# Kernel optimization log

Measured on AMD Instinct MI355X. Metric: run time of the kernel, lower is better.

## Reference

```python
import jax, jax.numpy as jnp
import numpy as np

N_ATOMS = 10000
N_PAIRS = 320000
C = 64        # channel width (pp_nodes[-1], ii_nodes[-1], pi_nodes[-1])
NB = 10       # n_basis
EPS = 1e-3    # torsion-boost epsilon


def setup_inputs() -> dict:
    key = jax.random.key(0)
    ks = jax.random.split(key, 24)
    f32 = jnp.float32

    def w(k, shp):
        return jax.random.normal(k, shp, f32) / np.float32(np.sqrt(shp[0]))

    ind_2 = jax.random.randint(ks[0], (N_PAIRS, 2), 0, N_ATOMS)
    p1 = jax.random.normal(ks[1], (N_ATOMS, C), f32)
    p3 = jax.random.normal(ks[2], (N_ATOMS, 3, C), f32)
    basis = jax.random.uniform(ks[3], (N_PAIRS, NB), dtype=f32)
    d3 = jax.random.normal(ks[4], (N_PAIRS, 3), f32)
    d3 = d3 / jnp.linalg.norm(d3, axis=-1, keepdims=True)  # unit bond directions
    fc_edge = jax.random.uniform(ks[5], (N_PAIRS, 1), dtype=f32)  # cutoff in [0,1]

    return {
        'ind_2': ind_2, 'p1': p1, 'p3': p3, 'basis': basis, 'd3': d3, 'fc_edge': fc_edge,
        'pp_pre_W1': w(ks[6], (C, C)), 'pp_pre_b1': jnp.zeros((C,), f32),
        'pp_pre_W2': w(ks[7], (C, C)), 'pp_pre_b2': jnp.zeros((C,), f32),
        'pi_W': w(ks[8], (2 * C, C * NB)), 'pi_b': jnp.zeros((C * NB,), f32),
        'ii_W': w(ks[9], (C, 2 * C)),
        'pp_post_W1': w(ks[10], (2 * C, C)), 'pp_post_W2': w(ks[11], (C, C)),
        'eq_pp_W': w(ks[12], (C, C)),
        'pp1_W1': w(ks[13], (2 * C, C)), 'pp1_b1': jnp.zeros((C,), f32),
        'pp1_W2': w(ks[14], (C, 2 * C)), 'pp1_b2': jnp.zeros((2 * C,), f32),
    }


def _gc_block(ind_2, p1, p3, basis, d3, fc_edge,
              pp_pre_W1, pp_pre_b1, pp_pre_W2, pp_pre_b2,
              pi_W, pi_b, ii_W, pp_post_W1, pp_post_W2,
              eq_pp_W, pp1_W1, pp1_b1, pp1_W2, pp1_b2):
    n_atoms = p1.shape[0]
    i = ind_2[:, 0]
    j = ind_2[:, 1]

    # ---- InvarLayer ----
    # pp_pre: FF [C,C], tanh, bias
    p1_in = jnp.tanh(jnp.tanh(p1 @ pp_pre_W1 + pp_pre_b1) @ pp_pre_W2 + pp_pre_b2)
    # PILayer: concat(p1[i], p1[j]) -> Dense(C*NB) -> contract with radial basis
    pair = jnp.concatenate([p1_in[i], p1_in[j]], axis=-1)            # (P, 2C)
    h = jnp.tanh(pair @ pi_W + pi_b).reshape(-1, C, NB)              # (P, C, NB)
    i_pair = jnp.einsum('pcb,pb->pc', h, basis)                      # (P, C)
    # ii: FF [2C] (doubled for n_props=2), tanh, no bias
    i_pair = jnp.tanh(i_pair @ ii_W)                                 # (P, 2C)
    # IP: scatter-add onto receiver atom i
    p1_scat = jax.ops.segment_sum(i_pair, i, num_segments=n_atoms)   # (N, 2C)
    # pp_post: FF [C,C], tanh, no bias
    p1_new = jnp.tanh(jnp.tanh(p1_scat @ pp_post_W1) @ pp_post_W2)   # (N, C)

    i1a, i1b = jnp.split(i_pair, 2, axis=-1)  # chunks; rank-3 branch uses i1s[1]

    # ---- torsion boost (compute_torsion_boost_t3) ----
    v = jax.ops.segment_sum(d3 * fc_edge, i, num_segments=n_atoms)   # (N, 3)
    v_i = v[i]
    proj = jnp.sum(v_i * d3, axis=-1, keepdims=True)
    w = v_i - proj * d3                                              # perpendicular part
    w2 = jnp.sum(w * w, axis=-1, keepdims=True)
    g_deg = w2 / (w2 + (10.0 * EPS) ** 2)
    t3 = w * jax.lax.rsqrt(w2 + EPS * EPS) * g_deg                   # (P, 3)
    tb_gate = g_deg * (fc_edge * fc_edge)                            # (P, 1)

    # ---- EquivarLayer ----
    gate = i1b[:, None, :]                                           # (P, 1, C)
    ix = p3[j] * gate + d3[:, :, None] * gate \
         + t3[:, :, None] * (i1b * tb_gate)[:, None, :]              # (P, 3, C)
    p3_new = jax.ops.segment_sum(ix, i, num_segments=n_atoms)        # (N, 3, C)
    p3_new = p3_new @ eq_pp_W                                        # PP: no bias, no act
    dotted = jnp.einsum('ixr,ixr->ir', p3_new, p3_new)               # (N, C)

    # ---- output PP + gating ----
    h2 = jnp.tanh(jnp.concatenate([p1_new, dotted], axis=-1) @ pp1_W1 + pp1_b1)
    h2 = jnp.tanh(h2 @ pp1_W2 + pp1_b2)                              # (N, 2C)
    g1, g3 = jnp.split(h2, 2, axis=-1)
    p1_out = g1                                                      # (N, C)
    p3_out = p3_new * g3[:, None, :]                                 # ScaleLayer
    return p1_out, p3_out


def reference(ind_2, p1, p3, basis, d3, fc_edge,
              pp_pre_W1, pp_pre_b1, pp_pre_W2, pp_pre_b2,
              pi_W, pi_b, ii_W, pp_post_W1, pp_post_W2,
              eq_pp_W, pp1_W1, pp1_b1, pp1_W2, pp1_b2):
    return _gc_block(ind_2, p1, p3, basis, d3, fc_edge,
                     pp_pre_W1, pp_pre_b1, pp_pre_W2, pp_pre_b2,
                     pi_W, pi_b, ii_W, pp_post_W1, pp_post_W2,
                     eq_pp_W, pp1_W1, pp1_b1, pp1_W2, pp1_b2)
```

## Files before the change

### kernel.cpp

```cpp
#include <hip/hip_runtime.h>
#include <hip/hip_bf16.h>

#define N_ATOMS 10000
#define N_PAIRS 320000
#define C_ 64
#define NB_ 10

typedef short bf16x8 __attribute__((ext_vector_type(8)));
typedef float f32x4 __attribute__((ext_vector_type(4)));

__device__ __forceinline__ float bf2f(__hip_bfloat16 x) { return __bfloat162float(x); }
__device__ __forceinline__ float ldf(const void* p, int i, int isf32) {
    return isf32 ? ((const float*)p)[i] : bf2f(((const __hip_bfloat16*)p)[i]);
}
__device__ __forceinline__ short f2bs(float x) {
    __hip_bfloat16 h = __float2bfloat16(x);
    return *reinterpret_cast<short*>(&h);
}
__device__ __forceinline__ float bs2f(unsigned short s) {
    return __uint_as_float(((unsigned)s) << 16);
}
__device__ __forceinline__ float tanh_fast(float x) {
    const float e = __expf(2.0f * x);
    return 1.0f - 2.0f * __builtin_amdgcn_rcpf(e + 1.0f);
}

#define W_PPREW1 0
#define W_PPREB1 4096
#define W_PPREW2 4160
#define W_PPREB2 8256
#define W_PIW    8320
#define W_PIB    90240
#define W_IIW    90880
#define W_PPOSTW1 99072
#define W_PPOSTW2 107264
#define W_EQW    111360
#define W_Q1W    115456
#define W_Q1B    123648
#define W_Q2W    123712
#define W_Q2B    131904
#define W_TOTAL  132032

__global__ void k_probe(const void* __restrict__ d3, int* __restrict__ flag)
{
    if (threadIdx.x == 0 && blockIdx.x == 0) {
        float sf = 0.f, sb = 0.f;
        const float* f = (const float*)d3;
        const __hip_bfloat16* b = (const __hip_bfloat16*)d3;
        for (int r = 0; r < 4; r++) {
            float x = f[r*3], y = f[r*3+1], z = f[r*3+2];
            float n = x*x + y*y + z*z;
            sf += isfinite(n) ? fabsf(n - 1.f) : 1e30f;
            float xb = bf2f(b[r*3]), yb = bf2f(b[r*3+1]), zb = bf2f(b[r*3+2]);
            float nb = xb*xb + yb*yb + zb*zb;
            sb += isfinite(nb) ? fabsf(nb - 1.f) : 1e30f;
        }
        *flag = (sf < sb) ? 1 : 0;
    }
}

__global__ __launch_bounds__(256) void k_convert(
    const void* s0, const void* s1, const void* s2, const void* s3,
    const void* s4, const void* s5, const void* s6, const void* s7,
    const void* s8, const void* s9, const void* s10, const void* s11,
    const void* s12, const void* s13,
    float* __restrict__ wbuf, const int* __restrict__ flagp)
{
    const int idx = blockIdx.x * 256 + threadIdx.x;
    if (idx >= W_TOTAL) return;
    const int isf32 = *flagp;
    const int offs[15] = {W_PPREW1, W_PPREB1, W_PPREW2, W_PPREB2, W_PIW, W_PIB,
                          W_IIW, W_PPOSTW1, W_PPOSTW2, W_EQW, W_Q1W, W_Q1B,
                          W_Q2W, W_Q2B, W_TOTAL};
    const void* srcs[14] = {s0,s1,s2,s3,s4,s5,s6,s7,s8,s9,s10,s11,s12,s13};
    int t = 0;
    while (idx >= offs[t + 1]) t++;
    wbuf[idx] = ldf(srcs[t], idx - offs[t], isf32);
}

__global__ __launch_bounds__(256) void k_pack(
    const float* __restrict__ wbuf,
    short* __restrict__ piWBh, short* __restrict__ piWBl,
    short* __restrict__ iiWh, short* __restrict__ iiWl)
{
    int idx = blockIdx.x * 256 + threadIdx.x;
    if (idx < 81920) {
        const int j = idx & 7, lane = (idx >> 3) & 63, s = (idx >> 9) & 3, T = idx >> 11;
        const int k = s * 32 + (lane >> 4) * 8 + j;
        const int colp = T * 16 + (lane & 15);
        const int b = colp >> 6, c = colp & 63;
        const float v = wbuf[W_PIW + k * 640 + c * 10 + b];
        const short hs = f2bs(v);
        piWBh[idx] = hs;
        piWBl[idx] = f2bs(v - bs2f((unsigned short)hs));
        return;
    }
    idx -= 81920;
    if (idx < 8192) {
        const int j = idx & 7, lane = (idx >> 3) & 63, s2 = (idx >> 9) & 1, ct = idx >> 10;
        const int k = s2 * 32 + (lane >> 4) * 8 + j;
        const int col = ct * 16 + (lane & 15);
        const float wv = wbuf[W_IIW + k * 128 + col];
        const short hs = f2bs(wv);
        iiWh[idx] = hs;
        iiWl[idx] = f2bs(wv - bs2f((unsigned short)hs));
    }
}

__global__ __launch_bounds__(256) void k_p1in(
    const void* __restrict__ p1, const float* __restrict__ wbuf,
    const int* __restrict__ flagp,
    unsigned short* __restrict__ p1h, unsigned short* __restrict__ p1l)
{
    const float* W1 = wbuf + W_PPREW1;
    const float* b1 = wbuf + W_PPREB1;
    const float* W2 = wbuf + W_PPREW2;
    const float* b2 = wbuf + W_PPREB2;
    const int isf32 = *flagp;
    __shared__ float x[4][C_];
    __shared__ float h[4][C_];
    const int t = threadIdx.x;
    const int slot = t >> 6, c = t & 63;
    const int atom = blockIdx.x * 4 + slot;
    x[slot][c] = ldf(p1, atom * C_ + c, isf32);
    __syncthreads();
    float acc = b1[c];
    for (int k = 0; k < C_; k++) acc += x[slot][k] * W1[k * C_ + c];
    h[slot][c] = tanh_fast(acc);
    __syncthreads();
    acc = b2[c];
    for (int k = 0; k < C_; k++) acc += h[slot][k] * W2[k * C_ + c];
    const float f = tanh_fast(acc);
    const short hs = f2bs(f);
    p1h[atom * C_ + c] = (unsigned short)hs;
    p1l[atom * C_ + c] = (unsigned short)f2bs(f - bs2f((unsigned short)hs));
}

__global__ __launch_bounds__(256) void k_hist(const int* __restrict__ ind2, int* __restrict__ cnt)
{
    const int p = blockIdx.x * 256 + threadIdx.x;
    if (p < N_PAIRS) atomicAdd(&cnt[ind2[2 * p]], 1);
}
__global__ __launch_bounds__(256) void k_scan(const int* __restrict__ cnt, int* __restrict__ offs)
{
    __shared__ int part[256];
    __shared__ int base[257];
    const int t = threadIdx.x;
    const int lo = t * 40, hi = (lo + 40 < N_ATOMS) ? lo + 40 : N_ATOMS;
    int s = 0;
    for (int b = lo; b < hi; b++) s += cnt[b];
    part[t] = s;
    __syncthreads();
    if (t == 0) {
        int run = 0;
        for (int i = 0; i < 256; i++) { base[i] = run; run += part[i]; }
        base[256] = run;
    }
    __syncthreads();
    int run = base[t];
    for (int b = lo; b < hi; b++) { offs[b] = run; run += cnt[b]; }
    if (t == 0) offs[N_ATOMS] = base[256];
}
__global__ __launch_bounds__(256) void k_cpcur(const int* __restrict__ offs, int* __restrict__ cur)
{
    const int i = blockIdx.x * 256 + threadIdx.x;
    if (i < N_ATOMS) cur[i] = offs[i];
}
__global__ __launch_bounds__(256) void k_scatter(const int* __restrict__ ind2,
                                                 int* __restrict__ cur, int* __restrict__ perm)
{
    const int p = blockIdx.x * 256 + threadIdx.x;
    if (p >= N_PAIRS) return;
    const int pos = atomicAdd(&cur[ind2[2 * p]], 1);
    perm[pos] = p;
}

__global__ __launch_bounds__(256) void k_vscat(
    const int* __restrict__ ind2, const void* __restrict__ d3,
    const void* __restrict__ fc, const int* __restrict__ flagp, float* __restrict__ v)
{
    const int p = blockIdx.x * 256 + threadIdx.x;
    if (p >= N_PAIRS) return;
    const int isf32 = *flagp;
    const int ia = ind2[2 * p];
    const float f = ldf(fc, p, isf32);
    atomicAdd(&v[ia * 3 + 0], ldf(d3, p * 3 + 0, isf32) * f);
    atomicAdd(&v[ia * 3 + 1], ldf(d3, p * 3 + 1, isf32) * f);
    atomicAdd(&v[ia * 3 + 2], ldf(d3, p * 3 + 2, isf32) * f);
}

template<int FULLMODE>
__global__ __launch_bounds__(256) void k_pairs_t(
    const int* __restrict__ ind2, const void* __restrict__ basis,
    const void* __restrict__ d3, const void* __restrict__ fc,
    const void* __restrict__ p3,
    const float* __restrict__ wbuf,
    const short* __restrict__ piWBh, const short* __restrict__ piWBl,
    const short* __restrict__ iiWh, const short* __restrict__ iiWl,
    const unsigned short* __restrict__ p1h, const unsigned short* __restrict__ p1l,
    const int* __restrict__ flagp, const float* __restrict__ vglob,
    float* __restrict__ outA, float* __restrict__ outB)
{
    __shared__ __align__(16) unsigned short Bbuf[8192];
    __shared__ __align__(16) char SH[17408];
    __shared__ float basisL[640];
    __shared__ int sIL[64], sJL[64];
    __shared__ float d3L[64][3], t3L[64][3], tbL[64];

    float* preL = (float*)SH;
    float* i1bL = (float*)SH;

    const int t = threadIdx.x;
    const int P0 = blockIdx.x * 64;
    const int isf32 = *flagp;
    const int lane = t & 63;
    const int w = t >> 6;
    const int lc = lane & 15;
    const int quad = lane >> 4;

    if (t < 64) {
        int2 ij = ((const int2*)ind2)[P0 + t];
        sIL[t] = ij.x; sJL[t] = ij.y;
    }
    for (int e = t; e < 640; e += 256) basisL[e] = ldf(basis, P0 * 10 + e, isf32);
    __syncthreads();

    bf16x8 ah[4], al[4];
    {
        const int ia = sIL[w * 16 + lc];
        const int ja = sJL[w * 16 + lc];
        #pragma unroll
        for (int s = 0; s < 4; s++) {
            const int atom = (s < 2) ? ia : ja;
            const int off = atom * 64 + (s & 1) * 32 + quad * 8;
            ah[s] = *(const bf16x8*)(p1h + off);
            al[s] = *(const bf16x8*)(p1l + off);
        }
    }

    float sr[4][4];
    #pragma unroll
    for (int r = 0; r < 4; r++)
        #pragma unroll
        for (int ph = 0; ph < 4; ph++) sr[r][ph] = 0.f;

    for (int cc = 0; cc < 10; cc++) {
        f32x4 acc[4];
        #pragma unroll
        for (int tt = 0; tt < 4; tt++) acc[tt] = (f32x4){0.f, 0.f, 0.f, 0.f};

        __syncthreads();
        {
            const uint4* gsrc = (const uint4*)(piWBh + cc * 8192);
            uint4* ldst = (uint4*)Bbuf;
            #pragma unroll
            for (int r = 0; r < 4; r++) ldst[r * 256 + t] = gsrc[r * 256 + t];
        }
        __syncthreads();
        #pragma unroll
        for (int tt = 0; tt < 4; tt++) {
            #pragma unroll
            for (int s = 0; s < 4; s++) {
                bf16x8 bfr = *(const bf16x8*)&Bbuf[((tt * 4 + s) * 64 + lane) * 8];
                acc[tt] = __builtin_amdgcn_mfma_f32_16x16x32_bf16(ah[s], bfr, acc[tt], 0, 0, 0);
                acc[tt] = __builtin_amdgcn_mfma_f32_16x16x32_bf16(al[s], bfr, acc[tt], 0, 0, 0);
            }
        }
        __syncthreads();
        {
            const uint4* gsrc = (const uint4*)(piWBl + cc * 8192);
            uint4* ldst = (uint4*)Bbuf;
            #pragma unroll
            for (int r = 0; r < 4; r++) ldst[r * 256 + t] = gsrc[r * 256 + t];
        }
        __syncthreads();
        #pragma unroll
        for (int tt = 0; tt < 4; tt++) {
            #pragma unroll
            for (int s = 0; s < 4; s++) {
                bf16x8 bfr = *(const bf16x8*)&Bbuf[((tt * 4 + s) * 64 + lane) * 8];
                acc[tt] = __builtin_amdgcn_mfma_f32_16x16x32_bf16(ah[s], bfr, acc[tt], 0, 0, 0);
            }
            const int c = tt * 16 + lc;
            const float bias = wbuf[W_PIB + c * 10 + cc];
            #pragma unroll
            for (int r = 0; r < 4; r++) {
                const int m = w * 16 + quad * 4 + r;
                const float h = tanh_fast(acc[tt][r] + bias);
                sr[r][tt] += h * basisL[m * 10 + cc];
            }
        }
    }

    #pragma unroll
    for (int r = 0; r < 4; r++)
        #pragma unroll
        for (int ph = 0; ph < 4; ph++)
            preL[(w * 16 + quad * 4 + r) * 68 + ph * 16 + lc] = sr[r][ph];
    __syncthreads();

    bf16x8 ah2[2], al2[2];
    {
        const int row = w * 16 + lc;
        #pragma unroll
        for (int s2 = 0; s2 < 2; s2++) {
            const float* pr2 = &preL[row * 68 + s2 * 32 + quad * 8];
            #pragma unroll
            for (int j = 0; j < 8; j++) {
                const float x = pr2[j];
                const short hs = f2bs(x);
                ah2[s2][j] = hs;
                al2[s2][j] = f2bs(x - bs2f((unsigned short)hs));
            }
        }
    }
    __syncthreads();

    #pragma unroll
    for (int ct = 0; ct < 8; ct++) {
        f32x4 acc = {0.f, 0.f, 0.f, 0.f};
        #pragma unroll
        for (int s2 = 0; s2 < 2; s2++) {
            bf16x8 bh = *(const bf16x8*)&iiWh[((ct * 2 + s2) * 64 + lane) * 8];
            bf16x8 bl = *(const bf16x8*)&iiWl[((ct * 2 + s2) * 64 + lane) * 8];
            acc = __builtin_amdgcn_mfma_f32_16x16x32_bf16(ah2[s2], bh, acc, 0, 0, 0);
            acc = __builtin_amdgcn_mfma_f32_16x16x32_bf16(al2[s2], bh, acc, 0, 0, 0);
            acc = __builtin_amdgcn_mfma_f32_16x16x32_bf16(ah2[s2], bl, acc, 0, 0, 0);
        }
        const int ch = ct * 16 + lc;
        if (FULLMODE) {
            #pragma unroll
            for (int r = 0; r < 4; r++) {
                const int m = w * 16 + quad * 4 + r;
                outA[(size_t)(P0 + m) * 128 + ch] = tanh_fast(acc[r]);
            }
        } else {
            #pragma unroll
            for (int r = 0; r < 4; r++) {
                const int m = w * 16 + quad * 4 + r;
                const float val = tanh_fast(acc[r]);
                atomicAdd(&outA[(size_t)sIL[m] * 128 + ch], val);
                if (ch >= 64) i1bL[m * 64 + (ch - 64)] = val;
            }
        }
    }

    if (!FULLMODE) {
        __syncthreads();
        if (t < 64) {
            const int m = t;
            const int ia = sIL[m];
            const float vi0 = vglob[ia * 3 + 0], vi1 = vglob[ia * 3 + 1], vi2 = vglob[ia * 3 + 2];
            const float d0 = ldf(d3, (P0 + m) * 3 + 0, isf32);
            const float d1 = ldf(d3, (P0 + m) * 3 + 1, isf32);
            const float d2 = ldf(d3, (P0 + m) * 3 + 2, isf32);
            d3L[m][0] = d0; d3L[m][1] = d1; d3L[m][2] = d2;
            const float proj = vi0 * d0 + vi1 * d1 + vi2 * d2;
            const float w0 = vi0 - proj * d0, w1 = vi1 - proj * d1, w2v = vi2 - proj * d2;
            const float w2 = w0 * w0 + w1 * w1 + w2v * w2v;
            const float g = w2 / (w2 + 1e-4f);
            const float rs = rsqrtf(w2 + 1e-6f);
            t3L[m][0] = w0 * rs * g; t3L[m][1] = w1 * rs * g; t3L[m][2] = w2v * rs * g;
            const float f = ldf(fc, P0 + m, isf32);
            tbL[m] = g * f * f;
        }
        __syncthreads();
        const int c = lane;
        #pragma unroll 4
        for (int mm = 0; mm < 16; mm++) {
            const int m = w * 16 + mm;
            const float bv = i1bL[m * 64 + c];
            const float coef = bv * tbL[m];
            #pragma unroll
            for (int x = 0; x < 3; x++) {
                const float p3v = ldf(p3, sJL[m] * 192 + x * 64 + c, isf32);
                atomicAdd(&outB[(size_t)sIL[m] * 192 + x * 64 + c],
                          p3v * bv + d3L[m][x] * bv + t3L[m][x] * coef);
            }
        }
    }
}

__global__ __launch_bounds__(64) void k_reduce(
    const int* __restrict__ ind2, const void* __restrict__ d3,
    const void* __restrict__ fc, const void* __restrict__ p3,
    const float* __restrict__ ip, const int* __restrict__ perm,
    const int* __restrict__ offs, const float* __restrict__ wbuf,
    const int* __restrict__ flagp, void* __restrict__ out)
{
    const int a = blockIdx.x;
    const int l = threadIdx.x;
    const int isf32 = *flagp;
    const int q0 = offs[a], q1 = offs[a + 1];

    float vx = 0.f, vy = 0.f, vz = 0.f;
    for (int q = q0 + l; q < q1; q += 64) {
        const int p = perm[q];
        const float f = ldf(fc, p, isf32);
        vx += ldf(d3, 3 * p + 0, isf32) * f;
        vy += ldf(d3, 3 * p + 1, isf32) * f;
        vz += ldf(d3, 3 * p + 2, isf32) * f;
    }
    #pragma unroll
    for (int off = 32; off; off >>= 1) {
        vx += __shfl_xor(vx, off);
        vy += __shfl_xor(vy, off);
        vz += __shfl_xor(vz, off);
    }

    float accA = 0.f, accB = 0.f, a30 = 0.f, a31 = 0.f, a32 = 0.f;
    #pragma unroll 2
    for (int q = q0; q < q1; q++) {
        const int p = perm[q];
        const float f = ldf(fc, p, isf32);
        const float d0 = ldf(d3, 3 * p + 0, isf32);
        const float d1 = ldf(d3, 3 * p + 1, isf32);
        const float d2 = ldf(d3, 3 * p + 2, isf32);
        const float proj = vx * d0 + vy * d1 + vz * d2;
        const float w0 = vx - proj * d0, w1 = vy - proj * d1, w2v = vz - proj * d2;
        const float w2 = w0 * w0 + w1 * w1 + w2v * w2v;
        const float g = w2 / (w2 + 1e-4f);
        const float rs = rsqrtf(w2 + 1e-6f);
        const float t30 = w0 * rs * g, t31 = w1 * rs * g, t32 = w2v * rs * g;
        const float tb = g * f * f;
        const int jj = ind2[2 * p + 1];
        const float ipa = ip[(size_t)p * 128 + l];
        const float ipb = ip[(size_t)p * 128 + 64 + l];
        accA += ipa; accB += ipb;
        const float coef = ipb * tb;
        a30 += ldf(p3, jj * 192 + l, isf32) * ipb + d0 * ipb + t30 * coef;
        a31 += ldf(p3, jj * 192 + 64 + l, isf32) * ipb + d1 * ipb + t31 * coef;
        a32 += ldf(p3, jj * 192 + 128 + l, isf32) * ipb + d2 * ipb + t32 * coef;
    }

    __shared__ float s1m[128];
    __shared__ float p3s[192];
    __shared__ float hA[64];
    __shared__ float cat[128];
    __shared__ float hB[64];
    s1m[l] = accA; s1m[64 + l] = accB;
    p3s[l] = a30; p3s[64 + l] = a31; p3s[128 + l] = a32;
    __syncthreads();

    const float* ppW1 = wbuf + W_PPOSTW1;
    const float* ppW2 = wbuf + W_PPOSTW2;
    const float* eqW  = wbuf + W_EQW;
    const float* q1W  = wbuf + W_Q1W;
    const float* q1b  = wbuf + W_Q1B;
    const float* q2W  = wbuf + W_Q2W;
    const float* q2b  = wbuf + W_Q2B;

    float acc = 0.f;
    for (int k = 0; k < 128; k++) acc += s1m[k] * ppW1[k * 64 + l];
    hA[l] = tanh_fast(acc);
    __syncthreads();
    acc = 0.f;
    for (int k = 0; k < 64; k++) acc += hA[k] * ppW2[k * 64 + l];
    const float p1n = tanh_fast(acc);

    float pn0 = 0.f, pn1 = 0.f, pn2 = 0.f;
    for (int k = 0; k < 64; k++) {
        const float e = eqW[k * 64 + l];
        pn0 += p3s[k] * e;
        pn1 += p3s[64 + k] * e;
        pn2 += p3s[128 + k] * e;
    }
    cat[l] = p1n;
    cat[64 + l] = pn0 * pn0 + pn1 * pn1 + pn2 * pn2;
    __syncthreads();

    acc = q1b[l];
    for (int k = 0; k < 128; k++) acc += cat[k] * q1W[k * 64 + l];
    hB[l] = tanh_fast(acc);
    __syncthreads();

    float g1 = q2b[l], g3 = q2b[64 + l];
    for (int k = 0; k < 64; k++) {
        const float hv = hB[k];
        g1 += hv * q2W[k * 128 + l];
        g3 += hv * q2W[k * 128 + 64 + l];
    }
    g1 = tanh_fast(g1);
    g3 = tanh_fast(g3);

    if (isf32) {
        float* p1o = (float*)out;
        float* p3o = p1o + 640000;
        p1o[a * 64 + l] = g1;
        p3o[a * 192 + l] = pn0 * g3;
        p3o[a * 192 + 64 + l] = pn1 * g3;
        p3o[a * 192 + 128 + l] = pn2 * g3;
    } else {
        __hip_bfloat16* p1o = (__hip_bfloat16*)out;
        __hip_bfloat16* p3o = p1o + 640000;
        p1o[a * 64 + l] = __float2bfloat16(g1);
        p3o[a * 192 + l] = __float2bfloat16(pn0 * g3);
        p3o[a * 192 + 64 + l] = __float2bfloat16(pn1 * g3);
        p3o[a * 192 + 128 + l] = __float2bfloat16(pn2 * g3);
    }
}

__global__ __launch_bounds__(256) void k_final(
    const float* __restrict__ p1scat, const float* __restrict__ p3acc,
    const float* __restrict__ wbuf, const int* __restrict__ flagp,
    void* __restrict__ out)
{
    const float* ppW1 = wbuf + W_PPOSTW1;
    const float* ppW2 = wbuf + W_PPOSTW2;
    const float* eqW  = wbuf + W_EQW;
    const float* q1W  = wbuf + W_Q1W;
    const float* q1b  = wbuf + W_Q1B;
    const float* q2W  = wbuf + W_Q2W;
    const float* q2b  = wbuf + W_Q2B;
    const int isf32 = *flagp;

    __shared__ float s1[4][128];
    __shared__ float hA[4][64];
    __shared__ float cat[4][128];
    __shared__ float p3a[4][192];
    const int t = threadIdx.x;
    const int slot = t >> 6, c = t & 63;
    const int atom = blockIdx.x * 4 + slot;

    s1[slot][c]        = p1scat[atom * 128 + c];
    s1[slot][64 + c]   = p1scat[atom * 128 + 64 + c];
    p3a[slot][c]       = p3acc[atom * 192 + c];
    p3a[slot][64 + c]  = p3acc[atom * 192 + 64 + c];
    p3a[slot][128 + c] = p3acc[atom * 192 + 128 + c];
    __syncthreads();

    float acc = 0.f;
    for (int k = 0; k < 128; k++) acc += s1[slot][k] * ppW1[k * 64 + c];
    hA[slot][c] = tanh_fast(acc);
    __syncthreads();
    acc = 0.f;
    for (int k = 0; k < 64; k++) acc += hA[slot][k] * ppW2[k * 64 + c];
    cat[slot][c] = tanh_fast(acc);

    float pn[3];
    float dot = 0.f;
    #pragma unroll
    for (int x = 0; x < 3; x++) {
        float a = 0.f;
        for (int k = 0; k < 64; k++) a += p3a[slot][x * 64 + k] * eqW[k * 64 + c];
        pn[x] = a;
        dot += a * a;
    }
    cat[slot][64 + c] = dot;
    __syncthreads();

    acc = q1b[c];
    for (int k = 0; k < 128; k++) acc += cat[slot][k] * q1W[k * 64 + c];
    __syncthreads();
    hA[slot][c] = tanh_fast(acc);
    __syncthreads();

    float g1acc = q2b[c], g3acc = q2b[c + 64];
    for (int k = 0; k < 64; k++) {
        const float hv = hA[slot][k];
        g1acc += hv * q2W[k * 128 + c];
        g3acc += hv * q2W[k * 128 + c + 64];
    }
    const float g1 = tanh_fast(g1acc);
    const float g3 = tanh_fast(g3acc);
    if (isf32) {
        float* p1o = (float*)out;
        float* p3o = p1o + 640000;
        p1o[atom * 64 + c] = g1;
        #pragma unroll
        for (int x = 0; x < 3; x++) p3o[atom * 192 + x * 64 + c] = pn[x] * g3;
    } else {
        __hip_bfloat16* p1o = (__hip_bfloat16*)out;
        __hip_bfloat16* p3o = p1o + 640000;
        p1o[atom * 64 + c] = __float2bfloat16(g1);
        #pragma unroll
        for (int x = 0; x < 3; x++) p3o[atom * 192 + x * 64 + c] = __float2bfloat16(pn[x] * g3);
    }
}

extern "C" void kernel_launch(void* const* d_in, const int* in_sizes, int n_in,
                              void* d_out, int out_size, void* d_ws, size_t ws_size,
                              hipStream_t stream)
{
    const int* ind2 = (const int*)d_in[0];
    const void* p1    = d_in[1];
    const void* p3    = d_in[2];
    const void* basis = d_in[3];
    const void* d3    = d_in[4];
    const void* fc    = d_in[5];

    char* W = (char*)d_ws;
    float* wbuf  = (float*)(W + 0);
    short* piWBh = (short*)(W + 528128);
    short* piWBl = (short*)(W + 691968);
    short* iiWh  = (short*)(W + 855808);
    short* iiWl  = (short*)(W + 872192);
    unsigned short* p1h = (unsigned short*)(W + 888576);
    unsigned short* p1l = (unsigned short*)(W + 2168576);
    int* flag = (int*)(W + 3448576);

    const int full = (ws_size >= 168688704ULL) ? 1 : 0;

    k_probe<<<1, 64, 0, stream>>>(d3, flag);
    k_convert<<<516, 256, 0, stream>>>(
        d_in[6], d_in[7], d_in[8], d_in[9], d_in[10], d_in[11], d_in[12],
        d_in[13], d_in[14], d_in[15], d_in[16], d_in[17], d_in[18], d_in[19],
        wbuf, flag);
    k_pack<<<352, 256, 0, stream>>>(wbuf, piWBh, piWBl, iiWh, iiWl);
    k_p1in<<<2500, 256, 0, stream>>>(p1, wbuf, flag, p1h, p1l);

    if (full) {
        int* cnt  = (int*)(W + 3448640);
        int* offs = (int*)(W + 3488640);
        int* cur  = (int*)(W + 3528704);
        int* perm = (int*)(W + 3568704);
        float* ip = (float*)(W + 4848704);

        hipMemsetAsync(cnt, 0, 40000, stream);
        k_hist<<<1250, 256, 0, stream>>>(ind2, cnt);
        k_scan<<<1, 256, 0, stream>>>(cnt, offs);
        k_cpcur<<<40, 256, 0, stream>>>(offs, cur);
        k_scatter<<<1250, 256, 0, stream>>>(ind2, cur, perm);
        k_pairs_t<1><<<5000, 256, 0, stream>>>(ind2, basis, d3, fc, p3,
                                               wbuf, piWBh, piWBl, iiWh, iiWl,
                                               p1h, p1l, flag, nullptr,
                                               ip, nullptr);
        k_reduce<<<10000, 64, 0, stream>>>(ind2, d3, fc, p3, ip, perm, offs,
                                           wbuf, flag, d_out);
    } else {
        float* v      = (float*)(W + 3448640);
        float* p1scat = (float*)(W + 3568640);
        float* p3acc  = (float*)(W + 8688640);

        hipMemsetAsync(v, 0, 120000 + 5120000 + 7680000, stream);
        k_vscat<<<1250, 256, 0, stream>>>(ind2, d3, fc, flag, v);
        k_pairs_t<0><<<5000, 256, 0, stream>>>(ind2, basis, d3, fc, p3,
                                               wbuf, piWBh, piWBl, iiWh, iiWl,
                                               p1h, p1l, flag, v,
                                               p1scat, p3acc);
        k_final<<<2500, 256, 0, stream>>>(p1scat, p3acc, wbuf, flag, d_out);
    }
}
```

Baseline: 528.3 us.

## Sort pairs by destination atom and pre-reduce runs before atomic scatter

Drops the two-mode path (full materialization plus per-atom reduce, or unsorted atomics) and always builds a counting-sort permutation of pairs by source atom. The vscat and pairs kernels process pairs in sorted order, so consecutive pairs share an atom; runs are summed in registers or shared memory and flushed with a single atomic per run instead of one per pair. This cuts atomic traffic to p1scat and p3acc and the size-dependent ip buffer, at the cost of the histogram, scan and scatter kernels and gathered reads of basis, d3 and fc through the permutation.

```diff
diff --git a/kernel.cpp b/kernel.cpp
--- a/kernel.cpp
+++ b/kernel.cpp
@@ -177,20 +177,34 @@
 
 __global__ __launch_bounds__(256) void k_vscat(
     const int* __restrict__ ind2, const void* __restrict__ d3,
-    const void* __restrict__ fc, const int* __restrict__ flagp, float* __restrict__ v)
-{
-    const int p = blockIdx.x * 256 + threadIdx.x;
-    if (p >= N_PAIRS) return;
+    const void* __restrict__ fc, const int* __restrict__ flagp,
+    const int* __restrict__ perm, float* __restrict__ v)
+{
+    __shared__ int iA[256];
+    __shared__ float sx[256], sy[256], sz[256];
+    const int t = threadIdx.x;
+    const int q = blockIdx.x * 256 + t;
     const int isf32 = *flagp;
+    const int p = perm[q];
     const int ia = ind2[2 * p];
     const float f = ldf(fc, p, isf32);
-    atomicAdd(&v[ia * 3 + 0], ldf(d3, p * 3 + 0, isf32) * f);
-    atomicAdd(&v[ia * 3 + 1], ldf(d3, p * 3 + 1, isf32) * f);
-    atomicAdd(&v[ia * 3 + 2], ldf(d3, p * 3 + 2, isf32) * f);
-}
-
-template<int FULLMODE>
-__global__ __launch_bounds__(256) void k_pairs_t(
+    iA[t] = ia;
+    sx[t] = ldf(d3, 3 * p + 0, isf32) * f;
+    sy[t] = ldf(d3, 3 * p + 1, isf32) * f;
+    sz[t] = ldf(d3, 3 * p + 2, isf32) * f;
+    __syncthreads();
+    const bool head = (t == 0) || (iA[t - 1] != ia);
+    if (head) {
+        float ax = sx[t], ay = sy[t], az = sz[t];
+        int m = t + 1;
+        while (m < 256 && iA[m] == ia) { ax += sx[m]; ay += sy[m]; az += sz[m]; m++; }
+        atomicAdd(&v[ia * 3 + 0], ax);
+        atomicAdd(&v[ia * 3 + 1], ay);
+        atomicAdd(&v[ia * 3 + 2], az);
+    }
+}
+
+__global__ __launch_bounds__(256) void k_pairs(
     const int* __restrict__ ind2, const void* __restrict__ basis,
     const void* __restrict__ d3, const void* __restrict__ fc,
     const void* __restrict__ p3,
@@ -199,16 +213,16 @@
     const short* __restrict__ iiWh, const short* __restrict__ iiWl,
     const unsigned short* __restrict__ p1h, const unsigned short* __restrict__ p1l,
     const int* __restrict__ flagp, const float* __restrict__ vglob,
-    float* __restrict__ outA, float* __restrict__ outB)
-{
-    __shared__ __align__(16) unsigned short Bbuf[8192];
-    __shared__ __align__(16) char SH[17408];
+    const int* __restrict__ perm,
+    float* __restrict__ p1scat, float* __restrict__ p3acc)
+{
+    __shared__ __align__(16) char U[33792];
+    unsigned short* Bbuf = (unsigned short*)U;
+    float* preL = (float*)(U + 16384);
+    float* ipL  = (float*)U;
     __shared__ float basisL[640];
-    __shared__ int sIL[64], sJL[64];
-    __shared__ float d3L[64][3], t3L[64][3], tbL[64];
-
-    float* preL = (float*)SH;
-    float* i1bL = (float*)SH;
+    __shared__ int pmL[64], sIL[64], sJL[64];
+    __shared__ float fcL[64], d3L[64][3], t3L[64][3], tbL[64];
 
     const int t = threadIdx.x;
     const int P0 = blockIdx.x * 64;
@@ -218,11 +232,21 @@
     const int lc = lane & 15;
     const int quad = lane >> 4;
 
+    if (t < 64) pmL[t] = perm[P0 + t];
+    __syncthreads();
     if (t < 64) {
-        int2 ij = ((const int2*)ind2)[P0 + t];
+        const int p = pmL[t];
+        int2 ij = ((const int2*)ind2)[p];
         sIL[t] = ij.x; sJL[t] = ij.y;
-    }
-    for (int e = t; e < 640; e += 256) basisL[e] = ldf(basis, P0 * 10 + e, isf32);
+        fcL[t] = ldf(fc, p, isf32);
+        d3L[t][0] = ldf(d3, 3 * p + 0, isf32);
+        d3L[t][1] = ldf(d3, 3 * p + 1, isf32);
+        d3L[t][2] = ldf(d3, 3 * p + 2, isf32);
+    }
+    for (int e = t; e < 640; e += 256) {
+        const int m = e / 10, b = e % 10;
+        basisL[e] = ldf(basis, pmL[m] * 10 + b, isf32);
+    }
     __syncthreads();
 
     bf16x8 ah[4], al[4];
@@ -292,6 +316,7 @@
         }
     }
 
+    __syncthreads();
     #pragma unroll
     for (int r = 0; r < 4; r++)
         #pragma unroll
@@ -328,175 +353,63 @@
             acc = __builtin_amdgcn_mfma_f32_16x16x32_bf16(ah2[s2], bl, acc, 0, 0, 0);
         }
         const int ch = ct * 16 + lc;
-        if (FULLMODE) {
-            #pragma unroll
-            for (int r = 0; r < 4; r++) {
-                const int m = w * 16 + quad * 4 + r;
-                outA[(size_t)(P0 + m) * 128 + ch] = tanh_fast(acc[r]);
-            }
-        } else {
-            #pragma unroll
-            for (int r = 0; r < 4; r++) {
-                const int m = w * 16 + quad * 4 + r;
-                const float val = tanh_fast(acc[r]);
-                atomicAdd(&outA[(size_t)sIL[m] * 128 + ch], val);
-                if (ch >= 64) i1bL[m * 64 + (ch - 64)] = val;
-            }
-        }
-    }
-
-    if (!FULLMODE) {
-        __syncthreads();
-        if (t < 64) {
-            const int m = t;
-            const int ia = sIL[m];
-            const float vi0 = vglob[ia * 3 + 0], vi1 = vglob[ia * 3 + 1], vi2 = vglob[ia * 3 + 2];
-            const float d0 = ldf(d3, (P0 + m) * 3 + 0, isf32);
-            const float d1 = ldf(d3, (P0 + m) * 3 + 1, isf32);
-            const float d2 = ldf(d3, (P0 + m) * 3 + 2, isf32);
-            d3L[m][0] = d0; d3L[m][1] = d1; d3L[m][2] = d2;
-            const float proj = vi0 * d0 + vi1 * d1 + vi2 * d2;
-            const float w0 = vi0 - proj * d0, w1 = vi1 - proj * d1, w2v = vi2 - proj * d2;
-            const float w2 = w0 * w0 + w1 * w1 + w2v * w2v;
-            const float g = w2 / (w2 + 1e-4f);
-            const float rs = rsqrtf(w2 + 1e-6f);
-            t3L[m][0] = w0 * rs * g; t3L[m][1] = w1 * rs * g; t3L[m][2] = w2v * rs * g;
-            const float f = ldf(fc, P0 + m, isf32);
-            tbL[m] = g * f * f;
-        }
-        __syncthreads();
-        const int c = lane;
-        #pragma unroll 4
-        for (int mm = 0; mm < 16; mm++) {
-            const int m = w * 16 + mm;
-            const float bv = i1bL[m * 64 + c];
-            const float coef = bv * tbL[m];
-            #pragma unroll
-            for (int x = 0; x < 3; x++) {
-                const float p3v = ldf(p3, sJL[m] * 192 + x * 64 + c, isf32);
-                atomicAdd(&outB[(size_t)sIL[m] * 192 + x * 64 + c],
-                          p3v * bv + d3L[m][x] * bv + t3L[m][x] * coef);
-            }
-        }
-    }
-}
-
-__global__ __launch_bounds__(64) void k_reduce(
-    const int* __restrict__ ind2, const void* __restrict__ d3,
-    const void* __restrict__ fc, const void* __restrict__ p3,
-    const float* __restrict__ ip, const int* __restrict__ perm,
-    const int* __restrict__ offs, const float* __restrict__ wbuf,
-    const int* __restrict__ flagp, void* __restrict__ out)
-{
-    const int a = blockIdx.x;
-    const int l = threadIdx.x;
-    const int isf32 = *flagp;
-    const int q0 = offs[a], q1 = offs[a + 1];
-
-    float vx = 0.f, vy = 0.f, vz = 0.f;
-    for (int q = q0 + l; q < q1; q += 64) {
-        const int p = perm[q];
-        const float f = ldf(fc, p, isf32);
-        vx += ldf(d3, 3 * p + 0, isf32) * f;
-        vy += ldf(d3, 3 * p + 1, isf32) * f;
-        vz += ldf(d3, 3 * p + 2, isf32) * f;
-    }
-    #pragma unroll
-    for (int off = 32; off; off >>= 1) {
-        vx += __shfl_xor(vx, off);
-        vy += __shfl_xor(vy, off);
-        vz += __shfl_xor(vz, off);
-    }
-
-    float accA = 0.f, accB = 0.f, a30 = 0.f, a31 = 0.f, a32 = 0.f;
-    #pragma unroll 2
-    for (int q = q0; q < q1; q++) {
-        const int p = perm[q];
-        const float f = ldf(fc, p, isf32);
-        const float d0 = ldf(d3, 3 * p + 0, isf32);
-        const float d1 = ldf(d3, 3 * p + 1, isf32);
-        const float d2 = ldf(d3, 3 * p + 2, isf32);
-        const float proj = vx * d0 + vy * d1 + vz * d2;
-        const float w0 = vx - proj * d0, w1 = vy - proj * d1, w2v = vz - proj * d2;
+        #pragma unroll
+        for (int r = 0; r < 4; r++) {
+            const int m = w * 16 + quad * 4 + r;
+            ipL[m * 132 + ch] = tanh_fast(acc[r]);
+        }
+    }
+    __syncthreads();
+
+    if (t < 64) {
+        const int m = t;
+        const int ia = sIL[m];
+        const float vi0 = vglob[ia * 3 + 0], vi1 = vglob[ia * 3 + 1], vi2 = vglob[ia * 3 + 2];
+        const float d0 = d3L[m][0], d1 = d3L[m][1], d2 = d3L[m][2];
+        const float proj = vi0 * d0 + vi1 * d1 + vi2 * d2;
+        const float w0 = vi0 - proj * d0, w1 = vi1 - proj * d1, w2v = vi2 - proj * d2;
         const float w2 = w0 * w0 + w1 * w1 + w2v * w2v;
         const float g = w2 / (w2 + 1e-4f);
         const float rs = rsqrtf(w2 + 1e-6f);
-        const float t30 = w0 * rs * g, t31 = w1 * rs * g, t32 = w2v * rs * g;
-        const float tb = g * f * f;
-        const int jj = ind2[2 * p + 1];
-        const float ipa = ip[(size_t)p * 128 + l];
-        const float ipb = ip[(size_t)p * 128 + 64 + l];
-        accA += ipa; accB += ipb;
-        const float coef = ipb * tb;
-        a30 += ldf(p3, jj * 192 + l, isf32) * ipb + d0 * ipb + t30 * coef;
-        a31 += ldf(p3, jj * 192 + 64 + l, isf32) * ipb + d1 * ipb + t31 * coef;
-        a32 += ldf(p3, jj * 192 + 128 + l, isf32) * ipb + d2 * ipb + t32 * coef;
-    }
-
-    __shared__ float s1m[128];
-    __shared__ float p3s[192];
-    __shared__ float hA[64];
-    __shared__ float cat[128];
-    __shared__ float hB[64];
-    s1m[l] = accA; s1m[64 + l] = accB;
-    p3s[l] = a30; p3s[64 + l] = a31; p3s[128 + l] = a32;
-    __syncthreads();
-
-    const float* ppW1 = wbuf + W_PPOSTW1;
-    const float* ppW2 = wbuf + W_PPOSTW2;
-    const float* eqW  = wbuf + W_EQW;
-    const float* q1W  = wbuf + W_Q1W;
-    const float* q1b  = wbuf + W_Q1B;
-    const float* q2W  = wbuf + W_Q2W;
-    const float* q2b  = wbuf + W_Q2B;
-
-    float acc = 0.f;
-    for (int k = 0; k < 128; k++) acc += s1m[k] * ppW1[k * 64 + l];
-    hA[l] = tanh_fast(acc);
-    __syncthreads();
-    acc = 0.f;
-    for (int k = 0; k < 64; k++) acc += hA[k] * ppW2[k * 64 + l];
-    const float p1n = tanh_fast(acc);
-
-    float pn0 = 0.f, pn1 = 0.f, pn2 = 0.f;
-    for (int k = 0; k < 64; k++) {
-        const float e = eqW[k * 64 + l];
-        pn0 += p3s[k] * e;
-        pn1 += p3s[64 + k] * e;
-        pn2 += p3s[128 + k] * e;
-    }
-    cat[l] = p1n;
-    cat[64 + l] = pn0 * pn0 + pn1 * pn1 + pn2 * pn2;
-    __syncthreads();
-
-    acc = q1b[l];
-    for (int k = 0; k < 128; k++) acc += cat[k] * q1W[k * 64 + l];
-    hB[l] = tanh_fast(acc);
-    __syncthreads();
-
-    float g1 = q2b[l], g3 = q2b[64 + l];
-    for (int k = 0; k < 64; k++) {
-        const float hv = hB[k];
-        g1 += hv * q2W[k * 128 + l];
-        g3 += hv * q2W[k * 128 + 64 + l];
-    }
-    g1 = tanh_fast(g1);
-    g3 = tanh_fast(g3);
-
-    if (isf32) {
-        float* p1o = (float*)out;
-        float* p3o = p1o + 640000;
-        p1o[a * 64 + l] = g1;
-        p3o[a * 192 + l] = pn0 * g3;
-        p3o[a * 192 + 64 + l] = pn1 * g3;
-        p3o[a * 192 + 128 + l] = pn2 * g3;
-    } else {
-        __hip_bfloat16* p1o = (__hip_bfloat16*)out;
-        __hip_bfloat16* p3o = p1o + 640000;
-        p1o[a * 64 + l] = __float2bfloat16(g1);
-        p3o[a * 192 + l] = __float2bfloat16(pn0 * g3);
-        p3o[a * 192 + 64 + l] = __float2bfloat16(pn1 * g3);
-        p3o[a * 192 + 128 + l] = __float2bfloat16(pn2 * g3);
+        t3L[m][0] = w0 * rs * g; t3L[m][1] = w1 * rs * g; t3L[m][2] = w2v * rs * g;
+        const float f = fcL[m];
+        tbL[m] = g * f * f;
+    }
+
+    {
+        const int ch = t & 127;
+        const int m0 = (t >> 7) * 32;
+        int cur = sIL[m0];
+        float acc = 0.f;
+        #pragma unroll 4
+        for (int m = m0; m < m0 + 32; m++) {
+            const int ia = sIL[m];
+            if (ia != cur) {
+                atomicAdd(&p1scat[(size_t)cur * 128 + ch], acc);
+                acc = 0.f; cur = ia;
+            }
+            acc += ipL[m * 132 + ch];
+        }
+        atomicAdd(&p1scat[(size_t)cur * 128 + ch], acc);
+    }
+    __syncthreads();
+
+    if (t < 192) {
+        const int x = t >> 6, c = t & 63;
+        int cur = sIL[0];
+        float acc = 0.f;
+        #pragma unroll 4
+        for (int m = 0; m < 64; m++) {
+            const int ia = sIL[m];
+            if (ia != cur) {
+                atomicAdd(&p3acc[(size_t)cur * 192 + x * 64 + c], acc);
+                acc = 0.f; cur = ia;
+            }
+            const float bv = ipL[m * 132 + 64 + c];
+            const float p3v = ldf(p3, sJL[m] * 192 + x * 64 + c, isf32);
+            acc += p3v * bv + d3L[m][x] * bv + t3L[m][x] * (bv * tbL[m]);
+        }
+        atomicAdd(&p3acc[(size_t)cur * 192 + x * 64 + c], acc);
     }
 }
 
@@ -597,9 +510,17 @@
     short* iiWl  = (short*)(W + 872192);
     unsigned short* p1h = (unsigned short*)(W + 888576);
     unsigned short* p1l = (unsigned short*)(W + 2168576);
-    int* flag = (int*)(W + 3448576);
-
-    const int full = (ws_size >= 168688704ULL) ? 1 : 0;
+    int*   flag  = (int*)(W + 3448576);
+    int*   cnt   = (int*)(W + 3448640);
+    int*   offs  = (int*)(W + 3488640);
+    int*   cur   = (int*)(W + 3528704);
+    int*   perm  = (int*)(W + 3568704);
+    float* v      = (float*)(W + 4848704);
+    float* p1scat = (float*)(W + 4968704);
+    float* p3acc  = (float*)(W + 10088704);
+
+    hipMemsetAsync(cnt, 0, 40000, stream);
+    hipMemsetAsync(v, 0, 120000 + 5120000 + 7680000, stream);
 
     k_probe<<<1, 64, 0, stream>>>(d3, flag);
     k_convert<<<516, 256, 0, stream>>>(
@@ -609,35 +530,15 @@
     k_pack<<<352, 256, 0, stream>>>(wbuf, piWBh, piWBl, iiWh, iiWl);
     k_p1in<<<2500, 256, 0, stream>>>(p1, wbuf, flag, p1h, p1l);
 
-    if (full) {
-        int* cnt  = (int*)(W + 3448640);
-        int* offs = (int*)(W + 3488640);
-        int* cur  = (int*)(W + 3528704);
-        int* perm = (int*)(W + 3568704);
-        float* ip = (float*)(W + 4848704);
-
-        hipMemsetAsync(cnt, 0, 40000, stream);
-        k_hist<<<1250, 256, 0, stream>>>(ind2, cnt);
-        k_scan<<<1, 256, 0, stream>>>(cnt, offs);
-        k_cpcur<<<40, 256, 0, stream>>>(offs, cur);
-        k_scatter<<<1250, 256, 0, stream>>>(ind2, cur, perm);
-        k_pairs_t<1><<<5000, 256, 0, stream>>>(ind2, basis, d3, fc, p3,
-                                               wbuf, piWBh, piWBl, iiWh, iiWl,
-                                               p1h, p1l, flag, nullptr,
-                                               ip, nullptr);
-        k_reduce<<<10000, 64, 0, stream>>>(ind2, d3, fc, p3, ip, perm, offs,
-                                           wbuf, flag, d_out);
-    } else {
-        float* v      = (float*)(W + 3448640);
-        float* p1scat = (float*)(W + 3568640);
-        float* p3acc  = (float*)(W + 8688640);
-
-        hipMemsetAsync(v, 0, 120000 + 5120000 + 7680000, stream);
-        k_vscat<<<1250, 256, 0, stream>>>(ind2, d3, fc, flag, v);
-        k_pairs_t<0><<<5000, 256, 0, stream>>>(ind2, basis, d3, fc, p3,
-                                               wbuf, piWBh, piWBl, iiWh, iiWl,
-                                               p1h, p1l, flag, v,
-                                               p1scat, p3acc);
-        k_final<<<2500, 256, 0, stream>>>(p1scat, p3acc, wbuf, flag, d_out);
-    }
-}
+    k_hist<<<1250, 256, 0, stream>>>(ind2, cnt);
+    k_scan<<<1, 256, 0, stream>>>(cnt, offs);
+    k_cpcur<<<40, 256, 0, stream>>>(offs, cur);
+    k_scatter<<<1250, 256, 0, stream>>>(ind2, cur, perm);
+    k_vscat<<<1250, 256, 0, stream>>>(ind2, d3, fc, flag, perm, v);
+
+    k_pairs<<<5000, 256, 0, stream>>>(ind2, basis, d3, fc, p3,
+                                      wbuf, piWBh, piWBl, iiWh, iiWl,
+                                      p1h, p1l, flag, v, perm,
+                                      p1scat, p3acc);
+    k_final<<<2500, 256, 0, stream>>>(p1scat, p3acc, wbuf, flag, d_out);
+}
```

Result: slower. 558.9 us (+5.8%).
